# Performance work log

Measured on AMD Instinct MI355X. Metric: run time of the kernel, lower is better.

Reference implementation:

```python
import jax, jax.numpy as jnp
import numpy as np
import math

D_MODEL = 1024
N_HEADS = 16
D_K = D_MODEL // N_HEADS


def setup_inputs() -> dict:
    key = jax.random.key(0)
    ks = jax.random.split(key, 5)
    std = math.sqrt(2.0 / (D_MODEL + D_MODEL))
    x = jax.random.normal(ks[0], (2, 2048, D_MODEL), dtype=jnp.float32)
    W_q = jax.random.normal(ks[1], (D_MODEL, D_MODEL), dtype=jnp.float32) * std
    W_k = jax.random.normal(ks[2], (D_MODEL, D_MODEL), dtype=jnp.float32) * std
    W_v = jax.random.normal(ks[3], (D_MODEL, D_MODEL), dtype=jnp.float32) * std
    W_o = jax.random.normal(ks[4], (D_MODEL, D_MODEL), dtype=jnp.float32) * std
    return {"x": x, "W_q": W_q, "W_k": W_k, "W_v": W_v, "W_o": W_o}


def reference(x, W_q, W_k, W_v, W_o):
    B, S, D = x.shape
    H, dk = N_HEADS, D_K
    # projections: (B,S,D) @ (D,D)
    def split_heads(t):  # (B,S,D) -> (B,H,S,dk)
        return t.reshape(B, S, H, dk).transpose(0, 2, 1, 3)
    Q = split_heads(x @ W_q)
    K = split_heads(x @ W_k)
    V = split_heads(x @ W_v)
    scale = 1.0 / math.sqrt(dk)
    scores = jnp.einsum("bhqd,bhkd->bhqk", Q, K) * scale  # (B,H,S,S)
    attn = jax.nn.softmax(scores, axis=-1)
    out = jnp.einsum("bhqk,bhkd->bhqd", attn, V)  # (B,H,S,dk)
    concat = out.transpose(0, 2, 1, 3).reshape(B, S, D)
    return concat @ W_o
```

## Files before the change

kernel.cpp:

```cpp
#include <hip/hip_runtime.h>
#include <hip/hip_bf16.h>
#include <math.h>

#define DMODEL 1024
#define NHEADS 16
#define DKH    64
#define BATCH  2
#define SEQ    2048
#define MROWS  (BATCH * SEQ)
#define LOG2E  1.4426950408889634f

typedef __bf16 bf16_t;
typedef bf16_t bf16x8 __attribute__((ext_vector_type(8)));
typedef bf16_t bf16x4 __attribute__((ext_vector_type(4)));
typedef float  floatx4 __attribute__((ext_vector_type(4)));

__device__ __forceinline__ void glds16(const bf16_t* g, bf16_t* l) {
    __builtin_amdgcn_global_load_lds((__attribute__((address_space(1))) unsigned*)(g),
                                     (__attribute__((address_space(3))) unsigned*)(l),
                                     16, 0, 0);
}

__global__ void cast_x_kernel(const float* __restrict__ x, bf16_t* __restrict__ xb) {
    int i = (blockIdx.x * 256 + threadIdx.x) * 4;
    float4 v = *(const float4*)(x + i);
    bf16_t o0 = (bf16_t)v.x, o1 = (bf16_t)v.y, o2 = (bf16_t)v.z, o3 = (bf16_t)v.w;
    bf16_t o[4] = {o0, o1, o2, o3};
    *(uint2*)(xb + i) = *(uint2*)o;
}

__global__ void transpose4_kernel(const float* __restrict__ W0, const float* __restrict__ W1,
                                  const float* __restrict__ W2, const float* __restrict__ W3,
                                  bf16_t* __restrict__ Wt) {
    __shared__ float t[32][33];
    const float* W = (blockIdx.z == 0) ? W0 : (blockIdx.z == 1) ? W1 : (blockIdx.z == 2) ? W2 : W3;
    bf16_t* dst = Wt + (size_t)blockIdx.z * DMODEL * DMODEL;
    int bx = blockIdx.x, by = blockIdx.y;
    int tx = threadIdx.x, ty = threadIdx.y;
#pragma unroll
    for (int i = 0; i < 32; i += 8)
        t[ty + i][tx] = W[(size_t)(by * 32 + ty + i) * DMODEL + bx * 32 + tx];
    __syncthreads();
#pragma unroll
    for (int i = 0; i < 32; i += 8)
        dst[(size_t)(bx * 32 + ty + i) * DMODEL + by * 32 + tx] = (bf16_t)t[tx][ty + i];
}

template<int MODE>
__global__ __launch_bounds__(256) void gemm128_kernel(const bf16_t* __restrict__ A,
                                                      const bf16_t* __restrict__ Bt,
                                                      void* __restrict__ outp) {
    __shared__ bf16_t As[128 * 64];
    __shared__ bf16_t Bs[128 * 64];
    int tid = threadIdx.x;
    int w = tid >> 6, l = tid & 63, g = l >> 4, lm = l & 15;
    int wr = w >> 1, wc = w & 1;
    int m0 = blockIdx.y * 128, n0 = blockIdx.x * 128;
    int r8 = l >> 3, s8 = l & 7, cw = s8 ^ r8;

    floatx4 acc[4][4];
#pragma unroll
    for (int i = 0; i < 4; ++i)
#pragma unroll
        for (int j = 0; j < 4; ++j) { floatx4 z = {0.f, 0.f, 0.f, 0.f}; acc[i][j] = z; }

    const bf16_t* Ag = A  + (size_t)(m0 + w * 32 + r8) * DMODEL + cw * 8;
    const bf16_t* Bg = Bt + (size_t)(n0 + w * 32 + r8) * DMODEL + cw * 8;

    for (int k0 = 0; k0 < DMODEL; k0 += 64) {
        __syncthreads();
#pragma unroll
        for (int j = 0; j < 4; ++j) {
            glds16(Ag + (size_t)j * 8 * DMODEL + k0, &As[(w * 32 + j * 8) * 64]);
            glds16(Bg + (size_t)j * 8 * DMODEL + k0, &Bs[(w * 32 + j * 8) * 64]);
        }
        __syncthreads();
#pragma unroll
        for (int kk = 0; kk < 2; ++kk) {
            bf16x8 af[4], bfr[4];
            int c = kk * 4 + g;
            int sw = (c ^ (lm & 7)) * 8;
#pragma unroll
            for (int i = 0; i < 4; ++i) {
                af[i]  = *(const bf16x8*)&As[(wr * 64 + i * 16 + lm) * 64 + sw];
                bfr[i] = *(const bf16x8*)&Bs[(wc * 64 + i * 16 + lm) * 64 + sw];
            }
#pragma unroll
            for (int i = 0; i < 4; ++i)
#pragma unroll
                for (int j = 0; j < 4; ++j)
                    acc[i][j] = __builtin_amdgcn_mfma_f32_16x16x32_bf16(af[i], bfr[j], acc[i][j], 0, 0, 0);
        }
    }

    const size_t NX = (size_t)MROWS * DMODEL;
#pragma unroll
    for (int i = 0; i < 4; ++i) {
#pragma unroll
        for (int j = 0; j < 4; ++j) {
            int nc = n0 + wc * 64 + j * 16 + lm;
            int mb = m0 + wr * 64 + i * 16 + g * 4;
            if (MODE == 0) {
                int mat = n0 >> 10;
                int col = nc & 1023;
                int hh = col >> 6, d = col & 63;
                int b = mb >> 11;
                int bh2 = b * NHEADS + hh;
                int s0 = mb & 2047;
                int kt = s0 >> 6;
                bf16_t* base = (bf16_t*)outp;
                if (mat == 0) {
#pragma unroll
                    for (int r = 0; r < 4; ++r)
                        base[((size_t)bh2 * SEQ + s0 + r) * DKH + d] = (bf16_t)(acc[i][j][r] * (0.125f * LOG2E));
                } else if (mat == 1) {
                    int kk = d >> 5, gK = (d >> 3) & 3, jK = d & 7;
                    int rt = s0 & 63, mt = rt >> 4, lmK = rt & 15;
                    bf16_t* Kfb = base + NX;
                    size_t tb = (((size_t)bh2 * 32 + kt) * 8 + mt * 2 + kk) * 512 + (gK * 16 + lmK) * 8 + jK;
#pragma unroll
                    for (int r = 0; r < 4; ++r)
                        Kfb[tb + (size_t)r * 8] = (bf16_t)acc[i][j][r];
                } else {
                    int dt = d >> 4, lmV = d & 15;
                    int s63 = s0 & 63;
                    int kkV = s63 >> 5, gV = (s63 >> 3) & 3, jV = s63 & 7;
                    bf16_t* Vfb = base + 2 * NX;
                    size_t tb = (((size_t)bh2 * 32 + kt) * 8 + dt * 2 + kkV) * 512 + (gV * 16 + lmV) * 8 + jV;
                    bf16x4 pk = {(bf16_t)acc[i][j][0], (bf16_t)acc[i][j][1],
                                 (bf16_t)acc[i][j][2], (bf16_t)acc[i][j][3]};
                    *(bf16x4*)&Vfb[tb] = pk;
                }
            } else {
#pragma unroll
                for (int r = 0; r < 4; ++r)
                    ((float*)outp)[(size_t)(mb + r) * DMODEL + nc] = acc[i][j][r];
            }
        }
    }
}

__global__ __launch_bounds__(256) void gemmO_kernel(const bf16_t* __restrict__ A,
                                                    const bf16_t* __restrict__ Bt,
                                                    float* __restrict__ outp) {
    __shared__ bf16_t As[64 * 64];
    __shared__ bf16_t Bs[128 * 64];
    int tid = threadIdx.x;
    int w = tid >> 6, l = tid & 63, g = l >> 4, lm = l & 15;
    int wr = w & 1, wc = w >> 1;
    int m0 = blockIdx.y * 64, n0 = blockIdx.x * 128;
    int r8 = l >> 3, s8 = l & 7, cw = s8 ^ r8;

    floatx4 acc[2][4];
#pragma unroll
    for (int i = 0; i < 2; ++i)
#pragma unroll
        for (int j = 0; j < 4; ++j) { floatx4 z = {0.f, 0.f, 0.f, 0.f}; acc[i][j] = z; }

    const bf16_t* Ag = A  + (size_t)(m0 + w * 16 + r8) * DMODEL + cw * 8;
    const bf16_t* Bg = Bt + (size_t)(n0 + w * 32 + r8) * DMODEL + cw * 8;

    for (int k0 = 0; k0 < DMODEL; k0 += 64) {
        __syncthreads();
#pragma unroll
        for (int j = 0; j < 2; ++j)
            glds16(Ag + (size_t)j * 8 * DMODEL + k0, &As[(w * 16 + j * 8) * 64]);
#pragma unroll
        for (int j = 0; j < 4; ++j)
            glds16(Bg + (size_t)j * 8 * DMODEL + k0, &Bs[(w * 32 + j * 8) * 64]);
        __syncthreads();
#pragma unroll
        for (int kk = 0; kk < 2; ++kk) {
            bf16x8 af[2], bfr[4];
            int c = kk * 4 + g;
            int sw = (c ^ (lm & 7)) * 8;
#pragma unroll
            for (int i = 0; i < 2; ++i)
                af[i] = *(const bf16x8*)&As[(wr * 32 + i * 16 + lm) * 64 + sw];
#pragma unroll
            for (int j = 0; j < 4; ++j)
                bfr[j] = *(const bf16x8*)&Bs[(wc * 64 + j * 16 + lm) * 64 + sw];
#pragma unroll
            for (int i = 0; i < 2; ++i)
#pragma unroll
                for (int j = 0; j < 4; ++j)
                    acc[i][j] = __builtin_amdgcn_mfma_f32_16x16x32_bf16(af[i], bfr[j], acc[i][j], 0, 0, 0);
        }
    }

#pragma unroll
    for (int i = 0; i < 2; ++i)
#pragma unroll
        for (int j = 0; j < 4; ++j) {
            int nc = n0 + wc * 64 + j * 16 + lm;
            int mb = m0 + wr * 32 + i * 16 + g * 4;
#pragma unroll
            for (int r = 0; r < 4; ++r)
                outp[(size_t)(mb + r) * DMODEL + nc] = acc[i][j][r];
        }
}

__global__ __launch_bounds__(256, 2) void attn_kernel(const bf16_t* __restrict__ Q,
                                                      const bf16_t* __restrict__ Kf,
                                                      const bf16_t* __restrict__ Vf,
                                                      bf16_t* __restrict__ Cc) {
    __shared__ __align__(16) char smem[37888];
    bf16_t* Ps   = (bf16_t*)smem;
    float*  Mbuf = (float*)smem;
    float*  Lbuf = (float*)(smem + 36864);

    int tid = threadIdx.x;
    int w = tid >> 6, l = tid & 63, g = l >> 4, lm = l & 15;
    int bh = blockIdx.x, b = bh >> 4, h = bh & 15;
    int q0 = blockIdx.y * 64;
    int xsw = lm & 14;

    const bf16_t* Qh  = Q  + ((size_t)bh * SEQ + q0) * DKH;
    const bf16_t* Kfh = Kf + (size_t)bh * 32 * 8 * 512 + l * 8;
    const bf16_t* Vfh = Vf + (size_t)bh * 32 * 8 * 512 + l * 8;

    bf16x8 qf[4][2];
#pragma unroll
    for (int nt = 0; nt < 4; ++nt)
#pragma unroll
        for (int kk = 0; kk < 2; ++kk)
            qf[nt][kk] = *(const bf16x8*)(Qh + (size_t)(nt * 16 + lm) * DKH + kk * 32 + g * 8);

    floatx4 oacc[4][4];
#pragma unroll
    for (int dt = 0; dt < 4; ++dt)
#pragma unroll
        for (int nt = 0; nt < 4; ++nt) { floatx4 z = {0.f, 0.f, 0.f, 0.f}; oacc[dt][nt] = z; }
    float lsum[4] = {0.f, 0.f, 0.f, 0.f};

    int kt0 = w * 8;
    bf16x8 kf[4][2], kfn[4][2], vf[4][2];
#pragma unroll
    for (int mt = 0; mt < 4; ++mt)
#pragma unroll
        for (int kk = 0; kk < 2; ++kk)
            kf[mt][kk] = *(const bf16x8*)(Kfh + ((size_t)kt0 * 8 + mt * 2 + kk) * 512);

#pragma unroll 2
    for (int it = 0; it < 8; ++it) {
        int kt = kt0 + it;
        const bf16_t* Vt = Vfh + (size_t)kt * 8 * 512;

#pragma unroll
        for (int dt = 0; dt < 4; ++dt)
#pragma unroll
            for (int kk = 0; kk < 2; ++kk)
                vf[dt][kk] = *(const bf16x8*)(Vt + (dt * 2 + kk) * 512);

        floatx4 sacc[4][4];
#pragma unroll
        for (int mt = 0; mt < 4; ++mt)
#pragma unroll
            for (int nt = 0; nt < 4; ++nt) { floatx4 z = {0.f, 0.f, 0.f, 0.f}; sacc[mt][nt] = z; }
#pragma unroll
        for (int kk = 0; kk < 2; ++kk)
#pragma unroll
            for (int mt = 0; mt < 4; ++mt)
#pragma unroll
                for (int nt = 0; nt < 4; ++nt)
                    sacc[mt][nt] = __builtin_amdgcn_mfma_f32_16x16x32_bf16(kf[mt][kk], qf[nt][kk], sacc[mt][nt], 0, 0, 0);

        int ktn = (it < 7) ? kt + 1 : kt0;
        const bf16_t* Kn = Kfh + (size_t)ktn * 8 * 512;
#pragma unroll
        for (int mt = 0; mt < 4; ++mt)
#pragma unroll
            for (int kk = 0; kk < 2; ++kk)
                kfn[mt][kk] = *(const bf16x8*)(Kn + (mt * 2 + kk) * 512);

#pragma unroll
        for (int mt = 0; mt < 4; ++mt)
#pragma unroll
            for (int nt = 0; nt < 4; ++nt) {
                float p0 = __builtin_amdgcn_exp2f(sacc[mt][nt][0]);
                float p1 = __builtin_amdgcn_exp2f(sacc[mt][nt][1]);
                float p2 = __builtin_amdgcn_exp2f(sacc[mt][nt][2]);
                float p3 = __builtin_amdgcn_exp2f(sacc[mt][nt][3]);
                lsum[nt] += (p0 + p1) + (p2 + p3);
                bf16x4 pk = {(bf16_t)p0, (bf16_t)p1, (bf16_t)p2, (bf16_t)p3};
                *(bf16x4*)&Ps[w * 4096 + (nt * 16 + lm) * 64 + (((mt * 4 + g) ^ xsw) << 2)] = pk;
            }

#pragma unroll
        for (int kk = 0; kk < 2; ++kk) {
            bf16x8 bp[4];
#pragma unroll
            for (int nt = 0; nt < 4; ++nt)
                bp[nt] = *(const bf16x8*)&Ps[w * 4096 + (nt * 16 + lm) * 64 + (((kk * 8 + g * 2) ^ xsw) << 2)];
#pragma unroll
            for (int dt = 0; dt < 4; ++dt)
#pragma unroll
                for (int nt = 0; nt < 4; ++nt)
                    oacc[dt][nt] = __builtin_amdgcn_mfma_f32_16x16x32_bf16(vf[dt][kk], bp[nt], oacc[dt][nt], 0, 0, 0);
        }

#pragma unroll
        for (int mt = 0; mt < 4; ++mt)
#pragma unroll
            for (int kk = 0; kk < 2; ++kk)
                kf[mt][kk] = kfn[mt][kk];
    }

#pragma unroll
    for (int nt = 0; nt < 4; ++nt) {
        float s = lsum[nt];
        s += __shfl_xor(s, 16, 64);
        s += __shfl_xor(s, 32, 64);
        lsum[nt] = s;
    }

    float linv = 0.f;
#pragma unroll
    for (int p = 0; p < 2; ++p) {
        __syncthreads();
#pragma unroll
        for (int dh = 0; dh < 2; ++dh) {
            int dt = p * 2 + dh;
#pragma unroll
            for (int nt = 0; nt < 4; ++nt)
                *(floatx4*)&Mbuf[w * 2304 + (nt * 16 + lm) * 36 + dh * 16 + g * 4] = oacc[dt][nt];
        }
        if (p == 0 && g == 0)
#pragma unroll
            for (int nt = 0; nt < 4; ++nt)
                Lbuf[w * 64 + nt * 16 + lm] = lsum[nt];
        __syncthreads();
        if (p == 0) {
            float lt = 0.f;
#pragma unroll
            for (int w2 = 0; w2 < 4; ++w2)
                lt += Lbuf[w2 * 64 + w * 16 + lm];
            linv = 1.0f / lt;
        }
#pragma unroll
        for (int cc = 0; cc < 2; ++cc) {
            floatx4 s = {0.f, 0.f, 0.f, 0.f};
#pragma unroll
            for (int w2 = 0; w2 < 4; ++w2)
                s += *(const floatx4*)&Mbuf[w2 * 2304 + (w * 16 + lm) * 36 + cc * 16 + g * 4];
            bf16x4 pk = {(bf16_t)(s[0] * linv), (bf16_t)(s[1] * linv),
                         (bf16_t)(s[2] * linv), (bf16_t)(s[3] * linv)};
            int q = q0 + w * 16 + lm;
            int d = h * DKH + p * 32 + cc * 16 + g * 4;
            *(bf16x4*)&Cc[((size_t)(b * SEQ + q)) * DMODEL + d] = pk;
        }
    }
}

extern "C" void kernel_launch(void* const* d_in, const int* in_sizes, int n_in,
                              void* d_out, int out_size, void* d_ws, size_t ws_size,
                              hipStream_t stream) {
    const float* x  = (const float*)d_in[0];
    const float* Wq = (const float*)d_in[1];
    const float* Wk = (const float*)d_in[2];
    const float* Wv = (const float*)d_in[3];
    const float* Wo = (const float*)d_in[4];

    const size_t NX = (size_t)MROWS * DMODEL;
    const size_t NW = (size_t)DMODEL * DMODEL;
    bf16_t* ws  = (bf16_t*)d_ws;
    bf16_t* xb  = ws;
    bf16_t* Wt  = xb + NX;
    bf16_t* Wto = Wt + 3 * NW;
    bf16_t* Qb  = Wt + 4 * NW;
    bf16_t* Kfb = Qb + NX;
    bf16_t* Vfb = Kfb + NX;
    bf16_t* Cc  = Vfb + NX;

    cast_x_kernel<<<NX / 1024, 256, 0, stream>>>(x, xb);
    transpose4_kernel<<<dim3(32, 32, 4), dim3(32, 8), 0, stream>>>(Wq, Wk, Wv, Wo, Wt);

    gemm128_kernel<0><<<dim3(3 * DMODEL / 128, MROWS / 128), 256, 0, stream>>>(xb, Wt, Qb);

    attn_kernel<<<dim3(BATCH * NHEADS, SEQ / 64), 256, 0, stream>>>(Qb, Kfb, Vfb, Cc);

    gemmO_kernel<<<dim3(DMODEL / 128, MROWS / 64), 256, 0, stream>>>(Cc, Wto, (float*)d_out);
}
```

Before: 195.4 us.

## Merge prep kernels, stage QKV epilogue through LDS, split attention K tiles

Folds the x cast into the weight transpose as one prep launch. The QKV GEMM epilogue now stages results in shared memory and writes Q/K/V with 16-byte coalesced stores instead of scattered 2-byte stores. The K/V fragment layout changes to 4096-element tiles. The attention loop splits each 64-key tile into two 32-key halves, which shrinks register pressure and the P buffer, and the output is staged through LDS for wide stores. The risks are extra syncs and LDS use, plus more serialised half-tile processing in attention.

```diff
diff --git a/kernel.cpp b/kernel.cpp
--- a/kernel.cpp
+++ b/kernel.cpp
@@ -21,22 +21,24 @@
                                      16, 0, 0);
 }
 
-__global__ void cast_x_kernel(const float* __restrict__ x, bf16_t* __restrict__ xb) {
-    int i = (blockIdx.x * 256 + threadIdx.x) * 4;
-    float4 v = *(const float4*)(x + i);
-    bf16_t o0 = (bf16_t)v.x, o1 = (bf16_t)v.y, o2 = (bf16_t)v.z, o3 = (bf16_t)v.w;
-    bf16_t o[4] = {o0, o1, o2, o3};
-    *(uint2*)(xb + i) = *(uint2*)o;
-}
-
-__global__ void transpose4_kernel(const float* __restrict__ W0, const float* __restrict__ W1,
-                                  const float* __restrict__ W2, const float* __restrict__ W3,
-                                  bf16_t* __restrict__ Wt) {
+__global__ void prep_kernel(const float* __restrict__ x,
+                            const float* __restrict__ W0, const float* __restrict__ W1,
+                            const float* __restrict__ W2, const float* __restrict__ W3,
+                            bf16_t* __restrict__ xb, bf16_t* __restrict__ Wt) {
     __shared__ float t[32][33];
-    const float* W = (blockIdx.z == 0) ? W0 : (blockIdx.z == 1) ? W1 : (blockIdx.z == 2) ? W2 : W3;
-    bf16_t* dst = Wt + (size_t)blockIdx.z * DMODEL * DMODEL;
-    int bx = blockIdx.x, by = blockIdx.y;
+    int bx = blockIdx.x, by = blockIdx.y, z = blockIdx.z;
     int tx = threadIdx.x, ty = threadIdx.y;
+    if (z == 0) {
+#pragma unroll
+        for (int k = 0; k < 16; ++k) {
+            int row = by * 128 + k * 8 + ty;
+            int col = bx * 32 + tx;
+            xb[(size_t)row * DMODEL + col] = (bf16_t)x[(size_t)row * DMODEL + col];
+        }
+        return;
+    }
+    const float* W = (z == 1) ? W0 : (z == 2) ? W1 : (z == 3) ? W2 : W3;
+    bf16_t* dst = Wt + (size_t)(z - 1) * DMODEL * DMODEL;
 #pragma unroll
     for (int i = 0; i < 32; i += 8)
         t[ty + i][tx] = W[(size_t)(by * 32 + ty + i) * DMODEL + bx * 32 + tx];
@@ -46,12 +48,14 @@
         dst[(size_t)(bx * 32 + ty + i) * DMODEL + by * 32 + tx] = (bf16_t)t[tx][ty + i];
 }
 
-template<int MODE>
-__global__ __launch_bounds__(256) void gemm128_kernel(const bf16_t* __restrict__ A,
-                                                      const bf16_t* __restrict__ Bt,
-                                                      void* __restrict__ outp) {
-    __shared__ bf16_t As[128 * 64];
-    __shared__ bf16_t Bs[128 * 64];
+__global__ __launch_bounds__(256) void gemm_qkv_kernel(const bf16_t* __restrict__ A,
+                                                       const bf16_t* __restrict__ Bt,
+                                                       bf16_t* __restrict__ Qb,
+                                                       bf16_t* __restrict__ Kfb,
+                                                       bf16_t* __restrict__ Vfb) {
+    __shared__ bf16_t sm[16384];
+    bf16_t* As = sm;
+    bf16_t* Bs = sm + 8192;
     int tid = threadIdx.x;
     int w = tid >> 6, l = tid & 63, g = l >> 4, lm = l & 15;
     int wr = w >> 1, wc = w & 1;
@@ -93,49 +97,74 @@
         }
     }
 
-    const size_t NX = (size_t)MROWS * DMODEL;
-#pragma unroll
-    for (int i = 0; i < 4; ++i) {
-#pragma unroll
-        for (int j = 0; j < 4; ++j) {
-            int nc = n0 + wc * 64 + j * 16 + lm;
-            int mb = m0 + wr * 64 + i * 16 + g * 4;
-            if (MODE == 0) {
-                int mat = n0 >> 10;
-                int col = nc & 1023;
-                int hh = col >> 6, d = col & 63;
-                int b = mb >> 11;
-                int bh2 = b * NHEADS + hh;
-                int s0 = mb & 2047;
-                int kt = s0 >> 6;
-                bf16_t* base = (bf16_t*)outp;
-                if (mat == 0) {
-#pragma unroll
-                    for (int r = 0; r < 4; ++r)
-                        base[((size_t)bh2 * SEQ + s0 + r) * DKH + d] = (bf16_t)(acc[i][j][r] * (0.125f * LOG2E));
-                } else if (mat == 1) {
-                    int kk = d >> 5, gK = (d >> 3) & 3, jK = d & 7;
-                    int rt = s0 & 63, mt = rt >> 4, lmK = rt & 15;
-                    bf16_t* Kfb = base + NX;
-                    size_t tb = (((size_t)bh2 * 32 + kt) * 8 + mt * 2 + kk) * 512 + (gK * 16 + lmK) * 8 + jK;
-#pragma unroll
-                    for (int r = 0; r < 4; ++r)
-                        Kfb[tb + (size_t)r * 8] = (bf16_t)acc[i][j][r];
-                } else {
-                    int dt = d >> 4, lmV = d & 15;
-                    int s63 = s0 & 63;
-                    int kkV = s63 >> 5, gV = (s63 >> 3) & 3, jV = s63 & 7;
-                    bf16_t* Vfb = base + 2 * NX;
-                    size_t tb = (((size_t)bh2 * 32 + kt) * 8 + dt * 2 + kkV) * 512 + (gV * 16 + lmV) * 8 + jV;
-                    bf16x4 pk = {(bf16_t)acc[i][j][0], (bf16_t)acc[i][j][1],
-                                 (bf16_t)acc[i][j][2], (bf16_t)acc[i][j][3]};
-                    *(bf16x4*)&Vfb[tb] = pk;
-                }
-            } else {
+    __syncthreads();
+    int mat = n0 >> 10;
+    int headb = (n0 & 1023) >> 6;
+    int b = m0 >> 11;
+    if (mat == 0) {
+#pragma unroll
+        for (int i = 0; i < 4; ++i)
+#pragma unroll
+            for (int j = 0; j < 4; ++j) {
+                int d = j * 16 + lm;
+                int so = wr * 64 + i * 16 + g * 4;
 #pragma unroll
                 for (int r = 0; r < 4; ++r)
-                    ((float*)outp)[(size_t)(mb + r) * DMODEL + nc] = acc[i][j][r];
-            }
+                    sm[wc * 8192 + (so + r) * 64 + d] = (bf16_t)(acc[i][j][r] * (0.125f * LOG2E));
+            }
+        __syncthreads();
+        int sbase = m0 & 2047;
+#pragma unroll
+        for (int rep = 0; rep < 8; ++rep) {
+            int idx = rep * 256 + tid;
+            int c = idx >> 10;
+            int off = (idx & 1023) * 8;
+            bf16_t* dst = Qb + ((size_t)(b * NHEADS + headb + c) * SEQ + sbase) * DKH + off;
+            *(bf16x8*)dst = *(const bf16x8*)&sm[c * 8192 + off];
+        }
+    } else if (mat == 1) {
+#pragma unroll
+        for (int i = 0; i < 4; ++i)
+#pragma unroll
+            for (int j = 0; j < 4; ++j) {
+                int d = j * 16 + lm;
+                int base = (wc * 2 + wr) * 4096 + (i * 2 + (d >> 5)) * 512 + ((d >> 3) & 3) * 128 + (d & 7);
+#pragma unroll
+                for (int r = 0; r < 4; ++r)
+                    sm[base + (g * 4 + r) * 8] = (bf16_t)acc[i][j][r];
+            }
+        __syncthreads();
+        int ktb = (m0 & 2047) >> 6;
+#pragma unroll
+        for (int rep = 0; rep < 8; ++rep) {
+            int idx = rep * 256 + tid;
+            int c = idx >> 9;
+            int off = (idx & 511) * 8;
+            int bh2 = b * NHEADS + headb + (c >> 1);
+            int kt = ktb + (c & 1);
+            *(bf16x8*)(Kfb + ((size_t)bh2 * 32 + kt) * 4096 + off) = *(const bf16x8*)&sm[c * 4096 + off];
+        }
+    } else {
+#pragma unroll
+        for (int i = 0; i < 4; ++i)
+#pragma unroll
+            for (int j = 0; j < 4; ++j) {
+                int base = (wc * 2 + wr) * 4096 + (j * 2 + (i >> 1)) * 512 +
+                           (((i & 1) * 2 + (g >> 1)) * 16 + lm) * 8 + (g & 1) * 4;
+                bf16x4 pk = {(bf16_t)acc[i][j][0], (bf16_t)acc[i][j][1],
+                             (bf16_t)acc[i][j][2], (bf16_t)acc[i][j][3]};
+                *(bf16x4*)&sm[base] = pk;
+            }
+        __syncthreads();
+        int ktb = (m0 & 2047) >> 6;
+#pragma unroll
+        for (int rep = 0; rep < 8; ++rep) {
+            int idx = rep * 256 + tid;
+            int c = idx >> 9;
+            int off = (idx & 511) * 8;
+            int bh2 = b * NHEADS + headb + (c >> 1);
+            int kt = ktb + (c & 1);
+            *(bf16x8*)(Vfb + ((size_t)bh2 * 32 + kt) * 4096 + off) = *(const bf16x8*)&sm[c * 4096 + off];
         }
     }
 }
@@ -204,20 +233,22 @@
                                                       const bf16_t* __restrict__ Kf,
                                                       const bf16_t* __restrict__ Vf,
                                                       bf16_t* __restrict__ Cc) {
-    __shared__ __align__(16) char smem[37888];
+    __shared__ __align__(16) char smem[41984];
     bf16_t* Ps   = (bf16_t*)smem;
     float*  Mbuf = (float*)smem;
     float*  Lbuf = (float*)(smem + 36864);
+    bf16_t* Ct   = (bf16_t*)(smem + 37888);
 
     int tid = threadIdx.x;
     int w = tid >> 6, l = tid & 63, g = l >> 4, lm = l & 15;
     int bh = blockIdx.x, b = bh >> 4, h = bh & 15;
     int q0 = blockIdx.y * 64;
-    int xsw = lm & 14;
+    int sw = lm & 6;
+    int s1 = sw >> 1;
 
     const bf16_t* Qh  = Q  + ((size_t)bh * SEQ + q0) * DKH;
-    const bf16_t* Kfh = Kf + (size_t)bh * 32 * 8 * 512 + l * 8;
-    const bf16_t* Vfh = Vf + (size_t)bh * 32 * 8 * 512 + l * 8;
+    const bf16_t* Kfh = Kf + (size_t)bh * 32 * 4096 + l * 8;
+    const bf16_t* Vfh = Vf + (size_t)bh * 32 * 4096 + l * 8;
 
     bf16x8 qf[4][2];
 #pragma unroll
@@ -234,76 +265,110 @@
     float lsum[4] = {0.f, 0.f, 0.f, 0.f};
 
     int kt0 = w * 8;
-    bf16x8 kf[4][2], kfn[4][2], vf[4][2];
-#pragma unroll
-    for (int mt = 0; mt < 4; ++mt)
+    bf16x8 kfa[2][2], kfb[2][2], vfa[4], vfb[4];
+    {
+        const bf16_t* Kb0 = Kfh + (size_t)kt0 * 4096;
+#pragma unroll
+        for (int m2 = 0; m2 < 2; ++m2)
+#pragma unroll
+            for (int kk = 0; kk < 2; ++kk)
+                kfa[m2][kk] = *(const bf16x8*)(Kb0 + (m2 * 2 + kk) * 512);
+    }
+
+    for (int it = 0; it < 8; ++it) {
+        const bf16_t* Tb = Kfh + (size_t)(kt0 + it) * 4096;
+        const bf16_t* Vb = Vfh + (size_t)(kt0 + it) * 4096;
+        const bf16_t* Tn = Kfh + (size_t)(kt0 + ((it < 7) ? it + 1 : 0)) * 4096;
+
+#pragma unroll
+        for (int dt = 0; dt < 4; ++dt) vfa[dt] = *(const bf16x8*)(Vb + (dt * 2 + 0) * 512);
+#pragma unroll
+        for (int m2 = 0; m2 < 2; ++m2)
+#pragma unroll
+            for (int kk = 0; kk < 2; ++kk)
+                kfb[m2][kk] = *(const bf16x8*)(Tb + (4 + m2 * 2 + kk) * 512);
+
+        floatx4 sa[2][4];
+#pragma unroll
+        for (int m2 = 0; m2 < 2; ++m2)
+#pragma unroll
+            for (int nt = 0; nt < 4; ++nt) { floatx4 z = {0.f, 0.f, 0.f, 0.f}; sa[m2][nt] = z; }
 #pragma unroll
         for (int kk = 0; kk < 2; ++kk)
-            kf[mt][kk] = *(const bf16x8*)(Kfh + ((size_t)kt0 * 8 + mt * 2 + kk) * 512);
-
-#pragma unroll 2
-    for (int it = 0; it < 8; ++it) {
-        int kt = kt0 + it;
-        const bf16_t* Vt = Vfh + (size_t)kt * 8 * 512;
-
-#pragma unroll
-        for (int dt = 0; dt < 4; ++dt)
+#pragma unroll
+            for (int m2 = 0; m2 < 2; ++m2)
+#pragma unroll
+                for (int nt = 0; nt < 4; ++nt)
+                    sa[m2][nt] = __builtin_amdgcn_mfma_f32_16x16x32_bf16(kfa[m2][kk], qf[nt][kk], sa[m2][nt], 0, 0, 0);
+
+#pragma unroll
+        for (int dt = 0; dt < 4; ++dt) vfb[dt] = *(const bf16x8*)(Vb + (dt * 2 + 1) * 512);
+#pragma unroll
+        for (int m2 = 0; m2 < 2; ++m2)
 #pragma unroll
             for (int kk = 0; kk < 2; ++kk)
-                vf[dt][kk] = *(const bf16x8*)(Vt + (dt * 2 + kk) * 512);
-
-        floatx4 sacc[4][4];
-#pragma unroll
-        for (int mt = 0; mt < 4; ++mt)
-#pragma unroll
-            for (int nt = 0; nt < 4; ++nt) { floatx4 z = {0.f, 0.f, 0.f, 0.f}; sacc[mt][nt] = z; }
+                kfa[m2][kk] = *(const bf16x8*)(Tn + (m2 * 2 + kk) * 512);
+
+        floatx4 sb[2][4];
+#pragma unroll
+        for (int m2 = 0; m2 < 2; ++m2)
+#pragma unroll
+            for (int nt = 0; nt < 4; ++nt) { floatx4 z = {0.f, 0.f, 0.f, 0.f}; sb[m2][nt] = z; }
 #pragma unroll
         for (int kk = 0; kk < 2; ++kk)
 #pragma unroll
-            for (int mt = 0; mt < 4; ++mt)
+            for (int m2 = 0; m2 < 2; ++m2)
 #pragma unroll
                 for (int nt = 0; nt < 4; ++nt)
-                    sacc[mt][nt] = __builtin_amdgcn_mfma_f32_16x16x32_bf16(kf[mt][kk], qf[nt][kk], sacc[mt][nt], 0, 0, 0);
-
-        int ktn = (it < 7) ? kt + 1 : kt0;
-        const bf16_t* Kn = Kfh + (size_t)ktn * 8 * 512;
-#pragma unroll
-        for (int mt = 0; mt < 4; ++mt)
-#pragma unroll
-            for (int kk = 0; kk < 2; ++kk)
-                kfn[mt][kk] = *(const bf16x8*)(Kn + (mt * 2 + kk) * 512);
-
-#pragma unroll
-        for (int mt = 0; mt < 4; ++mt)
+                    sb[m2][nt] = __builtin_amdgcn_mfma_f32_16x16x32_bf16(kfb[m2][kk], qf[nt][kk], sb[m2][nt], 0, 0, 0);
+
+#pragma unroll
+        for (int m2 = 0; m2 < 2; ++m2)
 #pragma unroll
             for (int nt = 0; nt < 4; ++nt) {
-                float p0 = __builtin_amdgcn_exp2f(sacc[mt][nt][0]);
-                float p1 = __builtin_amdgcn_exp2f(sacc[mt][nt][1]);
-                float p2 = __builtin_amdgcn_exp2f(sacc[mt][nt][2]);
-                float p3 = __builtin_amdgcn_exp2f(sacc[mt][nt][3]);
+                float p0 = __builtin_amdgcn_exp2f(sa[m2][nt][0]);
+                float p1 = __builtin_amdgcn_exp2f(sa[m2][nt][1]);
+                float p2 = __builtin_amdgcn_exp2f(sa[m2][nt][2]);
+                float p3 = __builtin_amdgcn_exp2f(sa[m2][nt][3]);
                 lsum[nt] += (p0 + p1) + (p2 + p3);
                 bf16x4 pk = {(bf16_t)p0, (bf16_t)p1, (bf16_t)p2, (bf16_t)p3};
-                *(bf16x4*)&Ps[w * 4096 + (nt * 16 + lm) * 64 + (((mt * 4 + g) ^ xsw) << 2)] = pk;
-            }
-
-#pragma unroll
-        for (int kk = 0; kk < 2; ++kk) {
+                *(bf16x4*)&Ps[w * 2048 + (nt * 16 + lm) * 32 + (((m2 * 4 + g) ^ sw) << 2)] = pk;
+            }
+        {
             bf16x8 bp[4];
 #pragma unroll
             for (int nt = 0; nt < 4; ++nt)
-                bp[nt] = *(const bf16x8*)&Ps[w * 4096 + (nt * 16 + lm) * 64 + (((kk * 8 + g * 2) ^ xsw) << 2)];
+                bp[nt] = *(const bf16x8*)&Ps[w * 2048 + (nt * 16 + lm) * 32 + ((g ^ s1) << 3)];
 #pragma unroll
             for (int dt = 0; dt < 4; ++dt)
 #pragma unroll
                 for (int nt = 0; nt < 4; ++nt)
-                    oacc[dt][nt] = __builtin_amdgcn_mfma_f32_16x16x32_bf16(vf[dt][kk], bp[nt], oacc[dt][nt], 0, 0, 0);
-        }
-
-#pragma unroll
-        for (int mt = 0; mt < 4; ++mt)
-#pragma unroll
-            for (int kk = 0; kk < 2; ++kk)
-                kf[mt][kk] = kfn[mt][kk];
+                    oacc[dt][nt] = __builtin_amdgcn_mfma_f32_16x16x32_bf16(vfa[dt], bp[nt], oacc[dt][nt], 0, 0, 0);
+        }
+
+#pragma unroll
+        for (int m2 = 0; m2 < 2; ++m2)
+#pragma unroll
+            for (int nt = 0; nt < 4; ++nt) {
+                float p0 = __builtin_amdgcn_exp2f(sb[m2][nt][0]);
+                float p1 = __builtin_amdgcn_exp2f(sb[m2][nt][1]);
+                float p2 = __builtin_amdgcn_exp2f(sb[m2][nt][2]);
+                float p3 = __builtin_amdgcn_exp2f(sb[m2][nt][3]);
+                lsum[nt] += (p0 + p1) + (p2 + p3);
+                bf16x4 pk = {(bf16_t)p0, (bf16_t)p1, (bf16_t)p2, (bf16_t)p3};
+                *(bf16x4*)&Ps[w * 2048 + (nt * 16 + lm) * 32 + (((m2 * 4 + g) ^ sw) << 2)] = pk;
+            }
+        {
+            bf16x8 bp[4];
+#pragma unroll
+            for (int nt = 0; nt < 4; ++nt)
+                bp[nt] = *(const bf16x8*)&Ps[w * 2048 + (nt * 16 + lm) * 32 + ((g ^ s1) << 3)];
+#pragma unroll
+            for (int dt = 0; dt < 4; ++dt)
+#pragma unroll
+                for (int nt = 0; nt < 4; ++nt)
+                    oacc[dt][nt] = __builtin_amdgcn_mfma_f32_16x16x32_bf16(vfb[dt], bp[nt], oacc[dt][nt], 0, 0, 0);
+        }
     }
 
 #pragma unroll
@@ -345,9 +410,12 @@
                 s += *(const floatx4*)&Mbuf[w2 * 2304 + (w * 16 + lm) * 36 + cc * 16 + g * 4];
             bf16x4 pk = {(bf16_t)(s[0] * linv), (bf16_t)(s[1] * linv),
                          (bf16_t)(s[2] * linv), (bf16_t)(s[3] * linv)};
-            int q = q0 + w * 16 + lm;
-            int d = h * DKH + p * 32 + cc * 16 + g * 4;
-            *(bf16x4*)&Cc[((size_t)(b * SEQ + q)) * DMODEL + d] = pk;
+            *(bf16x4*)&Ct[w * 512 + lm * 32 + cc * 16 + g * 4] = pk;
+        }
+        {
+            int row = l >> 2, dp = l & 3;
+            bf16x8 v = *(const bf16x8*)&Ct[w * 512 + row * 32 + dp * 8];
+            *(bf16x8*)&Cc[((size_t)(b * SEQ + q0 + w * 16 + row)) * DMODEL + h * DKH + p * 32 + dp * 8] = v;
         }
     }
 }
@@ -372,10 +440,9 @@
     bf16_t* Vfb = Kfb + NX;
     bf16_t* Cc  = Vfb + NX;
 
-    cast_x_kernel<<<NX / 1024, 256, 0, stream>>>(x, xb);
-    transpose4_kernel<<<dim3(32, 32, 4), dim3(32, 8), 0, stream>>>(Wq, Wk, Wv, Wo, Wt);
-
-    gemm128_kernel<0><<<dim3(3 * DMODEL / 128, MROWS / 128), 256, 0, stream>>>(xb, Wt, Qb);
+    prep_kernel<<<dim3(32, 32, 5), dim3(32, 8), 0, stream>>>(x, Wq, Wk, Wv, Wo, xb, Wt);
+
+    gemm_qkv_kernel<<<dim3(3 * DMODEL / 128, MROWS / 128), 256, 0, stream>>>(xb, Wt, Qb, Kfb, Vfb);
 
     attn_kernel<<<dim3(BATCH * NHEADS, SEQ / 64), 256, 0, stream>>>(Qb, Kfb, Vfb, Cc);
 
```

Result: faster. 177.7 us (-9.1%).
